# Kernel optimization log

Hardware: AMD Instinct MI355X
Metric: run time of the kernel (lower is better)

Reference implementation:

```python
import jax, jax.numpy as jnp
import numpy as np

B, T, C = 4, 2048, 1024
N_HEAD = 16
HEAD_DIM = C // N_HEAD


def setup_inputs() -> dict:
    key = jax.random.key(0)
    ks = jax.random.split(key, 5)
    s = 0.02
    return {
        "x": jax.random.normal(ks[0], (B, T, C), dtype=jnp.float32),
        "w_attn": jax.random.normal(ks[1], (C, 3 * C), dtype=jnp.float32) * s,
        "b_attn": jnp.zeros((3 * C,), dtype=jnp.float32),
        "w_proj": jax.random.normal(ks[2], (C, C), dtype=jnp.float32) * s,
        "b_proj": jnp.zeros((C,), dtype=jnp.float32),
    }


def reference(x, w_attn, b_attn, w_proj, b_proj):
    Bx, Tx, Cx = x.shape
    qkv = x @ w_attn + b_attn  # [B,T,3C]
    q, k, v = jnp.split(qkv, 3, axis=-1)
    # [B, H, T, D]
    q = q.reshape(Bx, Tx, N_HEAD, HEAD_DIM).transpose(0, 2, 1, 3)
    k = k.reshape(Bx, Tx, N_HEAD, HEAD_DIM).transpose(0, 2, 1, 3)
    v = v.reshape(Bx, Tx, N_HEAD, HEAD_DIM).transpose(0, 2, 1, 3)
    scale = 1.0 / np.sqrt(HEAD_DIM).astype(np.float32)
    att = jnp.einsum("bhqd,bhkd->bhqk", q, k) * scale  # [B,H,T,T]
    causal = jnp.tril(jnp.ones((Tx, Tx), dtype=bool))
    att = jnp.where(causal[None, None], att, jnp.float32(-jnp.inf))
    att = jax.nn.softmax(att, axis=-1)
    y = jnp.einsum("bhqk,bhkd->bhqd", att, v)  # [B,H,T,D]
    y = y.transpose(0, 2, 1, 3).reshape(Bx, Tx, Cx)
    return y @ w_proj + b_proj
```

## Files before the change

kernel.cpp:

```cpp
#include <hip/hip_runtime.h>
#include <hip/hip_bf16.h>

#define T_SEQ 2048
#define NHEAD 16
#define HDIM  64
#define CDIM  1024

typedef __attribute__((ext_vector_type(8))) short bf16x8;
typedef __attribute__((ext_vector_type(4))) short bf16x4;
typedef __attribute__((ext_vector_type(4))) float f32x4;

__device__ __forceinline__ unsigned short f2bf(float f) {
  union { __hip_bfloat16 h; unsigned short u; } c;
  c.h = __float2bfloat16(f);
  return c.u;
}

#define GLD16(g, l) __builtin_amdgcn_global_load_lds( \
  (const __attribute__((address_space(1))) void*)(g), \
  (__attribute__((address_space(3))) void*)(l), 16, 0, 0)

__global__ void cvt_bf16(const float* __restrict__ in, unsigned short* __restrict__ out, int n4) {
  const int i = blockIdx.x * 256 + threadIdx.x;
  if (i >= n4) return;
  const float4 v = ((const float4*)in)[i];
  ushort4 o;
  o.x = f2bf(v.x); o.y = f2bf(v.y); o.z = f2bf(v.z); o.w = f2bf(v.w);
  ((ushort4*)out)[i] = o;
}

__global__ void transpose_cvt(const float* __restrict__ in, unsigned short* __restrict__ out,
                              int R, int C) {
  __shared__ float tile[32][33];
  const int tx = threadIdx.x & 31, ty = threadIdx.x >> 5;
  const int c0 = blockIdx.x * 32, r0 = blockIdx.y * 32;
#pragma unroll
  for (int i = 0; i < 32; i += 8)
    tile[ty + i][tx] = in[(size_t)(r0 + ty + i) * C + c0 + tx];
  __syncthreads();
#pragma unroll
  for (int i = 0; i < 32; i += 8)
    out[(size_t)(c0 + ty + i) * R + r0 + tx] = f2bf(tile[tx][ty + i]);
}

template<int OUTF32>
__global__ __launch_bounds__(256, 2)
void gemm_bt(const unsigned short* __restrict__ A, const unsigned short* __restrict__ BT,
             const float* __restrict__ bias, void* __restrict__ outp,
             int M, int N, int K) {
  const int tid = threadIdx.x;
  const int w = tid >> 6, lane = tid & 63;
  const int lg = lane >> 4, l15 = lane & 15;
  const int wr = w >> 1, wc = w & 1;
  const int n0 = blockIdx.x * 128, m0 = blockIdx.y * 128;

  __shared__ unsigned short As[128 * 32];
  __shared__ unsigned short Bs[128 * 32];

  f32x4 acc[4][4] = {};

  for (int k0 = 0; k0 < K; k0 += 32) {
    __syncthreads();
#pragma unroll
    for (int i = 0; i < 2; ++i) {
      const int cb = i * 256 + w * 64;
      const int c  = cb + lane;
      const int row = c >> 2, slot = c & 3;
      GLD16(A  + (size_t)(m0 + row) * K + k0 + slot * 8, (char*)As + cb * 16);
      GLD16(BT + (size_t)(n0 + row) * K + k0 + slot * 8, (char*)Bs + cb * 16);
    }
    __syncthreads();
    bf16x8 af[4], bfr[4];
#pragma unroll
    for (int mt = 0; mt < 4; ++mt)
      af[mt] = *(const bf16x8*)&As[(wr * 64 + mt * 16 + l15) * 32 + lg * 8];
#pragma unroll
    for (int nt = 0; nt < 4; ++nt)
      bfr[nt] = *(const bf16x8*)&Bs[(wc * 64 + nt * 16 + l15) * 32 + lg * 8];
#pragma unroll
    for (int mt = 0; mt < 4; ++mt)
#pragma unroll
      for (int nt = 0; nt < 4; ++nt)
        acc[mt][nt] = __builtin_amdgcn_mfma_f32_16x16x32_bf16(af[mt], bfr[nt], acc[mt][nt], 0, 0, 0);
  }

#pragma unroll
  for (int mt = 0; mt < 4; ++mt) {
#pragma unroll
    for (int nt = 0; nt < 4; ++nt) {
      const int col = n0 + wc * 64 + nt * 16 + l15;
      const float bv = bias[col];
#pragma unroll
      for (int j = 0; j < 4; ++j) {
        const int row = m0 + wr * 64 + mt * 16 + lg * 4 + j;
        const float v = acc[mt][nt][j] + bv;
        if (OUTF32) ((float*)outp)[(size_t)row * N + col] = v;
        else ((unsigned short*)outp)[(size_t)row * N + col] = f2bf(v);
      }
    }
  }
}

#define EXPC 0.18033688f
__global__ __launch_bounds__(512, 4)
void attn_causal5(const unsigned short* __restrict__ qkv, unsigned short* __restrict__ att) {
  const int tid = threadIdx.x;
  const int w = tid >> 6, lane = tid & 63;
  const int lg = lane >> 4, l15 = lane & 15;

  const int fid = blockIdx.x;
  const int f2 = (fid & 7) * 64 + (fid >> 3);
  const int pair = f2 & 7, bh = f2 >> 3;
  const int b = bh >> 4, h = bh & 15;

  __shared__ unsigned short Kl[2][2][64][32];
  __shared__ unsigned short Vt[2][64][64];

  const unsigned short* base = qkv + (size_t)b * T_SEQ * 3072;

  auto STAGE_K = [&](int kv0, int buf) {
    const int c = tid;
    const int kc = c >> 8, slot = (c >> 2) & 63;
    const int s2 = (c & 3) ^ ((slot >> 1) & 3);
    const int v = (slot & 35) | ((slot & 8) << 1) | ((slot & 4) << 1) | ((slot & 16) >> 2);
    GLD16(base + (size_t)(kv0 + v) * 3072 + 1024 + h * 64 + kc * 32 + s2 * 8,
          (char*)&Kl[buf][0][0][0] + w * 1024);
  };

  bf16x4 vra, vrb;
  const int vkp = tid >> 4, vd4 = tid & 15;
  auto VLOAD = [&](int kv0) {
    const unsigned short* p = base + (size_t)(kv0 + 2 * vkp) * 3072 + 2048 + h * 64 + vd4 * 4;
    vra = *(const bf16x4*)p;
    vrb = *(const bf16x4*)(p + 3072);
  };
  auto VWRITE = [&](int buf) {
    const int ch = vkp >> 2, cl = (vkp & 3) * 2;
#pragma unroll
    for (int j = 0; j < 4; ++j) {
      const int r = vd4 * 4 + j;
      const unsigned int u = (unsigned short)vra[j] |
                             ((unsigned int)(unsigned short)vrb[j] << 16);
      *(unsigned int*)&Vt[buf][r][((ch ^ (r >> 3) ^ (r & 7)) << 3) + cl] = u;
    }
  };

  bf16x8 ones;
#pragma unroll
  for (int j = 0; j < 8; ++j) ones[j] = (short)0x3F80;

  for (int half = 0; half < 2; ++half) {
    const int qt = half ? (15 - pair) : pair;
    const int q0 = qt << 7;
    const int ntl = (qt + 1) << 1;
    const int qminS = __builtin_amdgcn_readfirstlane(q0 + w * 16);
    const int qme = qminS + l15;

    bf16x8 qf[2];
#pragma unroll
    for (int kc = 0; kc < 2; ++kc)
      qf[kc] = *(const bf16x8*)(base + (size_t)qme * 3072 + h * 64 + kc * 32 + lg * 8);

    f32x4 oacc[4] = {};
    f32x4 lsum = {};
    float m = -1e30f;

    STAGE_K(0, 0);
    VLOAD(0);
    VWRITE(0);
    __syncthreads();

    for (int t = 0; t < ntl; ++t) {
      const int cur = t & 1, nxt = cur ^ 1;
      const bool pf = (t + 1) < ntl;
      if (pf) { STAGE_K((t + 1) << 6, nxt); VLOAD((t + 1) << 6); }
      const int kv0 = t << 6;

      if (kv0 <= qminS + 15) {
        const int ksl = (lg ^ ((l15 >> 1) & 3)) * 8;
        f32x4 sc[4];
        __builtin_amdgcn_s_setprio(1);
#pragma unroll
        for (int kg = 0; kg < 4; ++kg) {
          f32x4 s = {};
#pragma unroll
          for (int kc = 0; kc < 2; ++kc) {
            bf16x8 kf = *(const bf16x8*)&Kl[cur][kc][kg * 16 + l15][ksl];
            s = __builtin_amdgcn_mfma_f32_16x16x32_bf16(kf, qf[kc], s, 0, 0, 0);
          }
          sc[kg] = s;
        }
        __builtin_amdgcn_s_setprio(0);

        float sv[4][4];
        if (kv0 + 63 > qminS) {
#pragma unroll
          for (int kg = 0; kg < 4; ++kg) {
            const int colb = kv0 + ((kg >> 1) << 5) + ((kg & 1) << 2) + lg * 8;
#pragma unroll
            for (int j = 0; j < 4; ++j)
              sv[kg][j] = (colb + j <= qme) ? sc[kg][j] : -1e30f;
          }
        } else {
#pragma unroll
          for (int kg = 0; kg < 4; ++kg)
#pragma unroll
            for (int j = 0; j < 4; ++j) sv[kg][j] = sc[kg][j];
        }

        float mx = -1e30f;
#pragma unroll
        for (int kg = 0; kg < 4; ++kg) {
          const float a = fmaxf(sv[kg][0], sv[kg][1]);
          const float c2 = fmaxf(sv[kg][2], sv[kg][3]);
          mx = fmaxf(mx, fmaxf(a, c2));
        }

        if (__any(mx > m + 55.4f)) {
          float mw = fmaxf(mx, __shfl_xor(mx, 16));
          mw = fmaxf(mw, __shfl_xor(mw, 32));
          const float mnew = fmaxf(m, mw);
          const float alc = exp2f((m - mnew) * EXPC);
          m = mnew;
          float alq[4];
#pragma unroll
          for (int j = 0; j < 4; ++j)
            alq[j] = __shfl(alc, (lane & 48) | (lg * 4 + j));
#pragma unroll
          for (int j = 0; j < 4; ++j) {
            lsum[j] *= alq[j];
#pragma unroll
            for (int dt = 0; dt < 4; ++dt) oacc[dt][j] *= alq[j];
          }
        }

        const float mc = m * EXPC;
        bf16x8 pa[2];
#pragma unroll
        for (int kg = 0; kg < 4; ++kg) {
          const int ks = kg >> 1, off = (kg & 1) * 4;
#pragma unroll
          for (int j = 0; j < 4; ++j) {
            const float p = exp2f(__fmaf_rn(sv[kg][j], EXPC, -mc));
            pa[ks][off + j] = (short)f2bf(p);
          }
        }

        __builtin_amdgcn_s_setprio(1);
        lsum = __builtin_amdgcn_mfma_f32_16x16x32_bf16(pa[0], ones, lsum, 0, 0, 0);
        lsum = __builtin_amdgcn_mfma_f32_16x16x32_bf16(pa[1], ones, lsum, 0, 0, 0);
#pragma unroll
        for (int dt = 0; dt < 4; ++dt) {
          f32x4 o = oacc[dt];
          const int d = dt * 16 + l15;
          const int gx = (d >> 3) ^ (d & 7);
#pragma unroll
          for (int ks = 0; ks < 2; ++ks) {
            bf16x8 vb = *(const bf16x8*)&Vt[cur][d][((ks * 4 + lg) ^ gx) << 3];
            o = __builtin_amdgcn_mfma_f32_16x16x32_bf16(pa[ks], vb, o, 0, 0, 0);
          }
          oacc[dt] = o;
        }
        __builtin_amdgcn_s_setprio(0);
      }

      if (pf) VWRITE(nxt);
      __syncthreads();
    }

#pragma unroll
    for (int dt = 0; dt < 4; ++dt)
#pragma unroll
      for (int j = 0; j < 4; ++j) {
        const int q = qminS + lg * 4 + j;
        att[(size_t)(b * T_SEQ + q) * CDIM + h * HDIM + dt * 16 + l15] =
            f2bf(oacc[dt][j] / lsum[j]);
      }
  }
}

extern "C" void kernel_launch(void* const* d_in, const int* in_sizes, int n_in,
                              void* d_out, int out_size, void* d_ws, size_t ws_size,
                              hipStream_t stream) {
  const float* x      = (const float*)d_in[0];
  const float* w_attn = (const float*)d_in[1];
  const float* b_attn = (const float*)d_in[2];
  const float* w_proj = (const float*)d_in[3];
  const float* b_proj = (const float*)d_in[4];

  char* ws = (char*)d_ws;
  unsigned short* xb  = (unsigned short*)(ws + 0);
  unsigned short* wat = (unsigned short*)(ws + 16777216);
  unsigned short* wpt = (unsigned short*)(ws + 23068672);
  unsigned short* qkv = (unsigned short*)(ws + 25165824);
  unsigned short* att = (unsigned short*)(ws + 75497472);

  cvt_bf16<<<8192, 256, 0, stream>>>(x, xb, 2097152);
  transpose_cvt<<<dim3(96, 32), 256, 0, stream>>>(w_attn, wat, 1024, 3072);
  transpose_cvt<<<dim3(32, 32), 256, 0, stream>>>(w_proj, wpt, 1024, 1024);
  gemm_bt<0><<<dim3(24, 64), 256, 0, stream>>>(xb, wat, b_attn, (void*)qkv, 8192, 3072, 1024);
  attn_causal5<<<dim3(512), 512, 0, stream>>>(qkv, att);
  gemm_bt<1><<<dim3(8, 64), 256, 0, stream>>>(att, wpt, b_proj, d_out, 8192, 1024, 1024);
}
```

Measured before the change: 187.6 us.

## Process two query row-tiles per wave in attention and swizzle GEMM block order

The attention kernel now runs 4 waves instead of 8, and each wave handles 32 query rows (two 16-row MFMA tiles). Each K and V fragment read from LDS is therefore reused for two MFMAs, and each thread stages twice as many K/V chunks. The GEMM remaps block indices with a stride-8 swizzle to improve L2 locality and raises its launch-bounds occupancy hint from 2 to 3. The trade-offs are more registers per wave and fewer waves per block to hide the softmax and load latency.

```diff
diff --git a/kernel.cpp b/kernel.cpp
--- a/kernel.cpp
+++ b/kernel.cpp
@@ -44,7 +44,7 @@
 }
 
 template<int OUTF32>
-__global__ __launch_bounds__(256, 2)
+__global__ __launch_bounds__(256, 3)
 void gemm_bt(const unsigned short* __restrict__ A, const unsigned short* __restrict__ BT,
              const float* __restrict__ bias, void* __restrict__ outp,
              int M, int N, int K) {
@@ -52,7 +52,11 @@
   const int w = tid >> 6, lane = tid & 63;
   const int lg = lane >> 4, l15 = lane & 15;
   const int wr = w >> 1, wc = w & 1;
-  const int n0 = blockIdx.x * 128, m0 = blockIdx.y * 128;
+
+  const int nb = gridDim.x * gridDim.y;
+  const int fid = blockIdx.y * gridDim.x + blockIdx.x;
+  const int swz = (fid & 7) * (nb >> 3) + (fid >> 3);
+  const int n0 = (swz % gridDim.x) * 128, m0 = (swz / gridDim.x) * 128;
 
   __shared__ unsigned short As[128 * 32];
   __shared__ unsigned short Bs[128 * 32];
@@ -102,8 +106,8 @@
 }
 
 #define EXPC 0.18033688f
-__global__ __launch_bounds__(512, 4)
-void attn_causal5(const unsigned short* __restrict__ qkv, unsigned short* __restrict__ att) {
+__global__ __launch_bounds__(256, 2)
+void attn_causal6(const unsigned short* __restrict__ qkv, unsigned short* __restrict__ att) {
   const int tid = threadIdx.x;
   const int w = tid >> 6, lane = tid & 63;
   const int lg = lane >> 4, l15 = lane & 15;
@@ -119,29 +123,39 @@
   const unsigned short* base = qkv + (size_t)b * T_SEQ * 3072;
 
   auto STAGE_K = [&](int kv0, int buf) {
-    const int c = tid;
-    const int kc = c >> 8, slot = (c >> 2) & 63;
-    const int s2 = (c & 3) ^ ((slot >> 1) & 3);
-    const int v = (slot & 35) | ((slot & 8) << 1) | ((slot & 4) << 1) | ((slot & 16) >> 2);
-    GLD16(base + (size_t)(kv0 + v) * 3072 + 1024 + h * 64 + kc * 32 + s2 * 8,
-          (char*)&Kl[buf][0][0][0] + w * 1024);
+#pragma unroll
+    for (int i = 0; i < 2; ++i) {
+      const int c = i * 256 + tid;
+      const int kc = c >> 8, slot = (c >> 2) & 63;
+      const int s2 = (c & 3) ^ ((slot >> 1) & 3);
+      const int v = (slot & 35) | ((slot & 8) << 1) | ((slot & 4) << 1) | ((slot & 16) >> 2);
+      GLD16(base + (size_t)(kv0 + v) * 3072 + 1024 + h * 64 + kc * 32 + s2 * 8,
+            (char*)&Kl[buf][0][0][0] + i * 4096 + w * 1024);
+    }
   };
 
-  bf16x4 vra, vrb;
-  const int vkp = tid >> 4, vd4 = tid & 15;
+  bf16x4 vra[2], vrb[2];
+  const int vkp0 = tid >> 4, vd4 = tid & 15;
   auto VLOAD = [&](int kv0) {
-    const unsigned short* p = base + (size_t)(kv0 + 2 * vkp) * 3072 + 2048 + h * 64 + vd4 * 4;
-    vra = *(const bf16x4*)p;
-    vrb = *(const bf16x4*)(p + 3072);
+#pragma unroll
+    for (int u = 0; u < 2; ++u) {
+      const unsigned short* p = base + (size_t)(kv0 + 2 * vkp0 + u * 32) * 3072 + 2048 + h * 64 + vd4 * 4;
+      vra[u] = *(const bf16x4*)p;
+      vrb[u] = *(const bf16x4*)(p + 3072);
+    }
   };
   auto VWRITE = [&](int buf) {
-    const int ch = vkp >> 2, cl = (vkp & 3) * 2;
-#pragma unroll
-    for (int j = 0; j < 4; ++j) {
-      const int r = vd4 * 4 + j;
-      const unsigned int u = (unsigned short)vra[j] |
-                             ((unsigned int)(unsigned short)vrb[j] << 16);
-      *(unsigned int*)&Vt[buf][r][((ch ^ (r >> 3) ^ (r & 7)) << 3) + cl] = u;
+#pragma unroll
+    for (int u = 0; u < 2; ++u) {
+      const int vkp = vkp0 + u * 16;
+      const int ch = vkp >> 2, cl = (vkp & 3) * 2;
+#pragma unroll
+      for (int j = 0; j < 4; ++j) {
+        const int r = vd4 * 4 + j;
+        const unsigned int pk = (unsigned short)vra[u][j] |
+                                ((unsigned int)(unsigned short)vrb[u][j] << 16);
+        *(unsigned int*)&Vt[buf][r][((ch ^ (r >> 3) ^ (r & 7)) << 3) + cl] = pk;
+      }
     }
   };
 
@@ -153,17 +167,19 @@
     const int qt = half ? (15 - pair) : pair;
     const int q0 = qt << 7;
     const int ntl = (qt + 1) << 1;
-    const int qminS = __builtin_amdgcn_readfirstlane(q0 + w * 16);
-    const int qme = qminS + l15;
-
-    bf16x8 qf[2];
-#pragma unroll
-    for (int kc = 0; kc < 2; ++kc)
-      qf[kc] = *(const bf16x8*)(base + (size_t)qme * 3072 + h * 64 + kc * 32 + lg * 8);
-
-    f32x4 oacc[4] = {};
-    f32x4 lsum = {};
-    float m = -1e30f;
+    const int qminS = __builtin_amdgcn_readfirstlane(q0 + w * 32);
+
+    bf16x8 qf[2][2];
+#pragma unroll
+    for (int qr = 0; qr < 2; ++qr)
+#pragma unroll
+      for (int kc = 0; kc < 2; ++kc)
+        qf[qr][kc] = *(const bf16x8*)(base + (size_t)(qminS + qr * 16 + l15) * 3072 +
+                                      h * 64 + kc * 32 + lg * 8);
+
+    f32x4 oacc[2][4] = {};
+    f32x4 lsum[2] = {};
+    float m[2] = {-1e30f, -1e30f};
 
     STAGE_K(0, 0);
     VLOAD(0);
@@ -176,90 +192,104 @@
       if (pf) { STAGE_K((t + 1) << 6, nxt); VLOAD((t + 1) << 6); }
       const int kv0 = t << 6;
 
-      if (kv0 <= qminS + 15) {
+      if (kv0 <= qminS + 31) {
         const int ksl = (lg ^ ((l15 >> 1) & 3)) * 8;
-        f32x4 sc[4];
+        f32x4 sc[2][4];
         __builtin_amdgcn_s_setprio(1);
 #pragma unroll
         for (int kg = 0; kg < 4; ++kg) {
-          f32x4 s = {};
+          f32x4 s0 = {}, s1 = {};
 #pragma unroll
           for (int kc = 0; kc < 2; ++kc) {
             bf16x8 kf = *(const bf16x8*)&Kl[cur][kc][kg * 16 + l15][ksl];
-            s = __builtin_amdgcn_mfma_f32_16x16x32_bf16(kf, qf[kc], s, 0, 0, 0);
-          }
-          sc[kg] = s;
+            s0 = __builtin_amdgcn_mfma_f32_16x16x32_bf16(kf, qf[0][kc], s0, 0, 0, 0);
+            s1 = __builtin_amdgcn_mfma_f32_16x16x32_bf16(kf, qf[1][kc], s1, 0, 0, 0);
+          }
+          sc[0][kg] = s0; sc[1][kg] = s1;
         }
         __builtin_amdgcn_s_setprio(0);
 
-        float sv[4][4];
         if (kv0 + 63 > qminS) {
 #pragma unroll
+          for (int qr = 0; qr < 2; ++qr) {
+            const int qme = qminS + qr * 16 + l15;
+#pragma unroll
+            for (int kg = 0; kg < 4; ++kg) {
+              const int colb = kv0 + ((kg >> 1) << 5) + ((kg & 1) << 2) + lg * 8;
+#pragma unroll
+              for (int j = 0; j < 4; ++j)
+                if (colb + j > qme) sc[qr][kg][j] = -1e30f;
+            }
+          }
+        }
+
+        float mx[2];
+#pragma unroll
+        for (int qr = 0; qr < 2; ++qr) {
+          float m1 = -1e30f;
+#pragma unroll
           for (int kg = 0; kg < 4; ++kg) {
-            const int colb = kv0 + ((kg >> 1) << 5) + ((kg & 1) << 2) + lg * 8;
+            const float a = fmaxf(sc[qr][kg][0], sc[qr][kg][1]);
+            const float c2 = fmaxf(sc[qr][kg][2], sc[qr][kg][3]);
+            m1 = fmaxf(m1, fmaxf(a, c2));
+          }
+          mx[qr] = m1;
+        }
+
+        if (__any(fmaxf(mx[0] - m[0], mx[1] - m[1]) > 55.4f)) {
+#pragma unroll
+          for (int qr = 0; qr < 2; ++qr) {
+            float mw = fmaxf(mx[qr], __shfl_xor(mx[qr], 16));
+            mw = fmaxf(mw, __shfl_xor(mw, 32));
+            const float mnew = fmaxf(m[qr], mw);
+            const float alc = exp2f((m[qr] - mnew) * EXPC);
+            m[qr] = mnew;
+            float alq[4];
 #pragma unroll
             for (int j = 0; j < 4; ++j)
-              sv[kg][j] = (colb + j <= qme) ? sc[kg][j] : -1e30f;
-          }
-        } else {
-#pragma unroll
-          for (int kg = 0; kg < 4; ++kg)
-#pragma unroll
-            for (int j = 0; j < 4; ++j) sv[kg][j] = sc[kg][j];
-        }
-
-        float mx = -1e30f;
-#pragma unroll
-        for (int kg = 0; kg < 4; ++kg) {
-          const float a = fmaxf(sv[kg][0], sv[kg][1]);
-          const float c2 = fmaxf(sv[kg][2], sv[kg][3]);
-          mx = fmaxf(mx, fmaxf(a, c2));
-        }
-
-        if (__any(mx > m + 55.4f)) {
-          float mw = fmaxf(mx, __shfl_xor(mx, 16));
-          mw = fmaxf(mw, __shfl_xor(mw, 32));
-          const float mnew = fmaxf(m, mw);
-          const float alc = exp2f((m - mnew) * EXPC);
-          m = mnew;
-          float alq[4];
-#pragma unroll
-          for (int j = 0; j < 4; ++j)
-            alq[j] = __shfl(alc, (lane & 48) | (lg * 4 + j));
-#pragma unroll
-          for (int j = 0; j < 4; ++j) {
-            lsum[j] *= alq[j];
-#pragma unroll
-            for (int dt = 0; dt < 4; ++dt) oacc[dt][j] *= alq[j];
-          }
-        }
-
-        const float mc = m * EXPC;
-        bf16x8 pa[2];
-#pragma unroll
-        for (int kg = 0; kg < 4; ++kg) {
-          const int ks = kg >> 1, off = (kg & 1) * 4;
-#pragma unroll
-          for (int j = 0; j < 4; ++j) {
-            const float p = exp2f(__fmaf_rn(sv[kg][j], EXPC, -mc));
-            pa[ks][off + j] = (short)f2bf(p);
+              alq[j] = __shfl(alc, (lane & 48) | (lg * 4 + j));
+#pragma unroll
+            for (int j = 0; j < 4; ++j) {
+              lsum[qr][j] *= alq[j];
+#pragma unroll
+              for (int dt = 0; dt < 4; ++dt) oacc[qr][dt][j] *= alq[j];
+            }
+          }
+        }
+
+        bf16x8 pa[2][2];
+#pragma unroll
+        for (int qr = 0; qr < 2; ++qr) {
+          const float mc = m[qr] * EXPC;
+#pragma unroll
+          for (int kg = 0; kg < 4; ++kg) {
+            const int ks = kg >> 1, off = (kg & 1) * 4;
+#pragma unroll
+            for (int j = 0; j < 4; ++j) {
+              const float p = exp2f(__fmaf_rn(sc[qr][kg][j], EXPC, -mc));
+              pa[qr][ks][off + j] = (short)f2bf(p);
+            }
           }
         }
 
         __builtin_amdgcn_s_setprio(1);
-        lsum = __builtin_amdgcn_mfma_f32_16x16x32_bf16(pa[0], ones, lsum, 0, 0, 0);
-        lsum = __builtin_amdgcn_mfma_f32_16x16x32_bf16(pa[1], ones, lsum, 0, 0, 0);
+#pragma unroll
+        for (int qr = 0; qr < 2; ++qr) {
+          lsum[qr] = __builtin_amdgcn_mfma_f32_16x16x32_bf16(pa[qr][0], ones, lsum[qr], 0, 0, 0);
+          lsum[qr] = __builtin_amdgcn_mfma_f32_16x16x32_bf16(pa[qr][1], ones, lsum[qr], 0, 0, 0);
+        }
 #pragma unroll
         for (int dt = 0; dt < 4; ++dt) {
-          f32x4 o = oacc[dt];
           const int d = dt * 16 + l15;
           const int gx = (d >> 3) ^ (d & 7);
+          f32x4 o0 = oacc[0][dt], o1 = oacc[1][dt];
 #pragma unroll
           for (int ks = 0; ks < 2; ++ks) {
             bf16x8 vb = *(const bf16x8*)&Vt[cur][d][((ks * 4 + lg) ^ gx) << 3];
-            o = __builtin_amdgcn_mfma_f32_16x16x32_bf16(pa[ks], vb, o, 0, 0, 0);
-          }
-          oacc[dt] = o;
+            o0 = __builtin_amdgcn_mfma_f32_16x16x32_bf16(pa[0][ks], vb, o0, 0, 0, 0);
+            o1 = __builtin_amdgcn_mfma_f32_16x16x32_bf16(pa[1][ks], vb, o1, 0, 0, 0);
+          }
+          oacc[0][dt] = o0; oacc[1][dt] = o1;
         }
         __builtin_amdgcn_s_setprio(0);
       }
@@ -269,13 +299,15 @@
     }
 
 #pragma unroll
-    for (int dt = 0; dt < 4; ++dt)
-#pragma unroll
-      for (int j = 0; j < 4; ++j) {
-        const int q = qminS + lg * 4 + j;
-        att[(size_t)(b * T_SEQ + q) * CDIM + h * HDIM + dt * 16 + l15] =
-            f2bf(oacc[dt][j] / lsum[j]);
-      }
+    for (int qr = 0; qr < 2; ++qr)
+#pragma unroll
+      for (int dt = 0; dt < 4; ++dt)
+#pragma unroll
+        for (int j = 0; j < 4; ++j) {
+          const int q = qminS + qr * 16 + lg * 4 + j;
+          att[(size_t)(b * T_SEQ + q) * CDIM + h * HDIM + dt * 16 + l15] =
+              f2bf(oacc[qr][dt][j] / lsum[qr][j]);
+        }
   }
 }
 
@@ -299,6 +331,6 @@
   transpose_cvt<<<dim3(96, 32), 256, 0, stream>>>(w_attn, wat, 1024, 3072);
   transpose_cvt<<<dim3(32, 32), 256, 0, stream>>>(w_proj, wpt, 1024, 1024);
   gemm_bt<0><<<dim3(24, 64), 256, 0, stream>>>(xb, wat, b_attn, (void*)qkv, 8192, 3072, 1024);
-  attn_causal5<<<dim3(512), 512, 0, stream>>>(qkv, att);
+  attn_causal6<<<dim3(512), 256, 0, stream>>>(qkv, att);
   gemm_bt<1><<<dim3(8, 64), 256, 0, stream>>>(att, wpt, b_proj, d_out, 8192, 1024, 1024);
 }
```

Result: no change. 188.2 us (+0.3%).

## Widen attention KV tile to 128, swizzle GEMM block order, raise occupancy

Applied to the files above, without the earlier changes.

The attention kernel now processes 128 KV positions per iteration instead of 64. This halves the loop trips and barriers and drops the per-tile skip check. The K and V LDS buffers are doubled, with an adjusted swizzle, and the causal mask applies only on the diagonal tile. Some waves now compute fully masked blocks, and the larger LDS footprint may limit occupancy. Separately, the GEMM remaps block indices for L2 locality, raises its launch-bounds occupancy hint to 3, and the final normalization uses a reciprocal instead of a divide.

```diff
diff --git a/kernel.cpp b/kernel.cpp
--- a/kernel.cpp
+++ b/kernel.cpp
@@ -44,7 +44,7 @@
 }
 
 template<int OUTF32>
-__global__ __launch_bounds__(256, 2)
+__global__ __launch_bounds__(256, 3)
 void gemm_bt(const unsigned short* __restrict__ A, const unsigned short* __restrict__ BT,
              const float* __restrict__ bias, void* __restrict__ outp,
              int M, int N, int K) {
@@ -52,7 +52,11 @@
   const int w = tid >> 6, lane = tid & 63;
   const int lg = lane >> 4, l15 = lane & 15;
   const int wr = w >> 1, wc = w & 1;
-  const int n0 = blockIdx.x * 128, m0 = blockIdx.y * 128;
+
+  const int nb = gridDim.x * gridDim.y;
+  const int fid = blockIdx.y * gridDim.x + blockIdx.x;
+  const int swz = (fid & 7) * (nb >> 3) + (fid >> 3);
+  const int n0 = (swz % gridDim.x) * 128, m0 = (swz / gridDim.x) * 128;
 
   __shared__ unsigned short As[128 * 32];
   __shared__ unsigned short Bs[128 * 32];
@@ -103,7 +107,7 @@
 
 #define EXPC 0.18033688f
 __global__ __launch_bounds__(512, 4)
-void attn_causal5(const unsigned short* __restrict__ qkv, unsigned short* __restrict__ att) {
+void attn_causal9(const unsigned short* __restrict__ qkv, unsigned short* __restrict__ att) {
   const int tid = threadIdx.x;
   const int w = tid >> 6, lane = tid & 63;
   const int lg = lane >> 4, l15 = lane & 15;
@@ -113,35 +117,46 @@
   const int pair = f2 & 7, bh = f2 >> 3;
   const int b = bh >> 4, h = bh & 15;
 
-  __shared__ unsigned short Kl[2][2][64][32];
-  __shared__ unsigned short Vt[2][64][64];
+  __shared__ unsigned short Kl[2][2][128][32];
+  __shared__ unsigned short Vt[2][64][128];
 
   const unsigned short* base = qkv + (size_t)b * T_SEQ * 3072;
 
   auto STAGE_K = [&](int kv0, int buf) {
-    const int c = tid;
-    const int kc = c >> 8, slot = (c >> 2) & 63;
-    const int s2 = (c & 3) ^ ((slot >> 1) & 3);
-    const int v = (slot & 35) | ((slot & 8) << 1) | ((slot & 4) << 1) | ((slot & 16) >> 2);
-    GLD16(base + (size_t)(kv0 + v) * 3072 + 1024 + h * 64 + kc * 32 + s2 * 8,
-          (char*)&Kl[buf][0][0][0] + w * 1024);
+#pragma unroll
+    for (int i = 0; i < 2; ++i) {
+      const int c = i * 512 + tid;
+      const int kc = c >> 9, slot = (c >> 2) & 127;
+      const int s2 = (c & 3) ^ ((slot >> 1) & 3);
+      const int v = (slot & 99) | ((slot & 8) << 1) | ((slot & 4) << 1) | ((slot & 16) >> 2);
+      GLD16(base + (size_t)(kv0 + v) * 3072 + 1024 + h * 64 + kc * 32 + s2 * 8,
+            (char*)&Kl[buf][0][0][0] + i * 8192 + w * 1024);
+    }
   };
 
-  bf16x4 vra, vrb;
-  const int vkp = tid >> 4, vd4 = tid & 15;
+  bf16x4 vra[2], vrb[2];
+  const int vkp0 = tid >> 4, vd4 = tid & 15;
   auto VLOAD = [&](int kv0) {
-    const unsigned short* p = base + (size_t)(kv0 + 2 * vkp) * 3072 + 2048 + h * 64 + vd4 * 4;
-    vra = *(const bf16x4*)p;
-    vrb = *(const bf16x4*)(p + 3072);
+#pragma unroll
+    for (int uu = 0; uu < 2; ++uu) {
+      const unsigned short* p = base + (size_t)(kv0 + 2 * (vkp0 + 32 * uu)) * 3072 + 2048 + h * 64 + vd4 * 4;
+      vra[uu] = *(const bf16x4*)p;
+      vrb[uu] = *(const bf16x4*)(p + 3072);
+    }
   };
   auto VWRITE = [&](int buf) {
-    const int ch = vkp >> 2, cl = (vkp & 3) * 2;
-#pragma unroll
-    for (int j = 0; j < 4; ++j) {
-      const int r = vd4 * 4 + j;
-      const unsigned int u = (unsigned short)vra[j] |
-                             ((unsigned int)(unsigned short)vrb[j] << 16);
-      *(unsigned int*)&Vt[buf][r][((ch ^ (r >> 3) ^ (r & 7)) << 3) + cl] = u;
+#pragma unroll
+    for (int uu = 0; uu < 2; ++uu) {
+      const int p2 = vkp0 + 32 * uu;
+      const int ch = p2 >> 2, cl = (p2 & 3) * 2;
+#pragma unroll
+      for (int j = 0; j < 4; ++j) {
+        const int r = vd4 * 4 + j;
+        const int phys = (ch & 8) | ((ch ^ (r >> 3) ^ (r & 7)) & 7);
+        const unsigned int pk = (unsigned short)vra[uu][j] |
+                                ((unsigned int)(unsigned short)vrb[uu][j] << 16);
+        *(unsigned int*)&Vt[buf][r][phys * 8 + cl] = pk;
+      }
     }
   };
 
@@ -152,7 +167,7 @@
   for (int half = 0; half < 2; ++half) {
     const int qt = half ? (15 - pair) : pair;
     const int q0 = qt << 7;
-    const int ntl = (qt + 1) << 1;
+    const int ntl = qt + 1;
     const int qminS = __builtin_amdgcn_readfirstlane(q0 + w * 16);
     const int qme = qminS + l15;
 
@@ -173,108 +188,106 @@
     for (int t = 0; t < ntl; ++t) {
       const int cur = t & 1, nxt = cur ^ 1;
       const bool pf = (t + 1) < ntl;
-      if (pf) { STAGE_K((t + 1) << 6, nxt); VLOAD((t + 1) << 6); }
-      const int kv0 = t << 6;
-
-      if (kv0 <= qminS + 15) {
-        const int ksl = (lg ^ ((l15 >> 1) & 3)) * 8;
-        f32x4 sc[4];
-        __builtin_amdgcn_s_setprio(1);
-#pragma unroll
-        for (int kg = 0; kg < 4; ++kg) {
-          f32x4 s = {};
-#pragma unroll
-          for (int kc = 0; kc < 2; ++kc) {
-            bf16x8 kf = *(const bf16x8*)&Kl[cur][kc][kg * 16 + l15][ksl];
-            s = __builtin_amdgcn_mfma_f32_16x16x32_bf16(kf, qf[kc], s, 0, 0, 0);
-          }
-          sc[kg] = s;
-        }
-        __builtin_amdgcn_s_setprio(0);
-
-        float sv[4][4];
-        if (kv0 + 63 > qminS) {
-#pragma unroll
-          for (int kg = 0; kg < 4; ++kg) {
-            const int colb = kv0 + ((kg >> 1) << 5) + ((kg & 1) << 2) + lg * 8;
-#pragma unroll
-            for (int j = 0; j < 4; ++j)
-              sv[kg][j] = (colb + j <= qme) ? sc[kg][j] : -1e30f;
-          }
-        } else {
-#pragma unroll
-          for (int kg = 0; kg < 4; ++kg)
-#pragma unroll
-            for (int j = 0; j < 4; ++j) sv[kg][j] = sc[kg][j];
-        }
-
-        float mx = -1e30f;
-#pragma unroll
-        for (int kg = 0; kg < 4; ++kg) {
-          const float a = fmaxf(sv[kg][0], sv[kg][1]);
-          const float c2 = fmaxf(sv[kg][2], sv[kg][3]);
-          mx = fmaxf(mx, fmaxf(a, c2));
-        }
-
-        if (__any(mx > m + 55.4f)) {
-          float mw = fmaxf(mx, __shfl_xor(mx, 16));
-          mw = fmaxf(mw, __shfl_xor(mw, 32));
-          const float mnew = fmaxf(m, mw);
-          const float alc = exp2f((m - mnew) * EXPC);
-          m = mnew;
-          float alq[4];
+      if (pf) { STAGE_K((t + 1) << 7, nxt); VLOAD((t + 1) << 7); }
+      const int kv0 = t << 7;
+
+      const int ksl = (lg ^ ((l15 >> 1) & 3)) * 8;
+      f32x4 sc[8];
+      __builtin_amdgcn_s_setprio(1);
+#pragma unroll
+      for (int kg = 0; kg < 8; ++kg) {
+        f32x4 s = {};
+#pragma unroll
+        for (int kc = 0; kc < 2; ++kc) {
+          bf16x8 kf = *(const bf16x8*)&Kl[cur][kc][kg * 16 + l15][ksl];
+          s = __builtin_amdgcn_mfma_f32_16x16x32_bf16(kf, qf[kc], s, 0, 0, 0);
+        }
+        sc[kg] = s;
+      }
+      __builtin_amdgcn_s_setprio(0);
+
+      if (t == qt) {
+#pragma unroll
+        for (int kg = 0; kg < 8; ++kg) {
+          const int colb = kv0 + ((kg >> 1) << 5) + ((kg & 1) << 2) + lg * 8;
 #pragma unroll
           for (int j = 0; j < 4; ++j)
-            alq[j] = __shfl(alc, (lane & 48) | (lg * 4 + j));
-#pragma unroll
-          for (int j = 0; j < 4; ++j) {
-            lsum[j] *= alq[j];
-#pragma unroll
-            for (int dt = 0; dt < 4; ++dt) oacc[dt][j] *= alq[j];
-          }
-        }
-
-        const float mc = m * EXPC;
-        bf16x8 pa[2];
-#pragma unroll
-        for (int kg = 0; kg < 4; ++kg) {
-          const int ks = kg >> 1, off = (kg & 1) * 4;
-#pragma unroll
-          for (int j = 0; j < 4; ++j) {
-            const float p = exp2f(__fmaf_rn(sv[kg][j], EXPC, -mc));
-            pa[ks][off + j] = (short)f2bf(p);
-          }
-        }
-
-        __builtin_amdgcn_s_setprio(1);
-        lsum = __builtin_amdgcn_mfma_f32_16x16x32_bf16(pa[0], ones, lsum, 0, 0, 0);
-        lsum = __builtin_amdgcn_mfma_f32_16x16x32_bf16(pa[1], ones, lsum, 0, 0, 0);
-#pragma unroll
-        for (int dt = 0; dt < 4; ++dt) {
-          f32x4 o = oacc[dt];
-          const int d = dt * 16 + l15;
-          const int gx = (d >> 3) ^ (d & 7);
-#pragma unroll
-          for (int ks = 0; ks < 2; ++ks) {
-            bf16x8 vb = *(const bf16x8*)&Vt[cur][d][((ks * 4 + lg) ^ gx) << 3];
-            o = __builtin_amdgcn_mfma_f32_16x16x32_bf16(pa[ks], vb, o, 0, 0, 0);
-          }
-          oacc[dt] = o;
-        }
-        __builtin_amdgcn_s_setprio(0);
-      }
+            if (colb + j > qme) sc[kg][j] = -1e30f;
+        }
+      }
+
+      float mx = -1e30f;
+#pragma unroll
+      for (int kg = 0; kg < 8; ++kg) {
+        const float a = fmaxf(sc[kg][0], sc[kg][1]);
+        const float c2 = fmaxf(sc[kg][2], sc[kg][3]);
+        mx = fmaxf(mx, fmaxf(a, c2));
+      }
+
+      if (__any(mx > m + 55.4f)) {
+        float mw = fmaxf(mx, __shfl_xor(mx, 16));
+        mw = fmaxf(mw, __shfl_xor(mw, 32));
+        const float mnew = fmaxf(m, mw);
+        const float alc = exp2f((m - mnew) * EXPC);
+        m = mnew;
+        float alq[4];
+#pragma unroll
+        for (int j = 0; j < 4; ++j)
+          alq[j] = __shfl(alc, (lane & 48) | (lg * 4 + j));
+#pragma unroll
+        for (int j = 0; j < 4; ++j) {
+          lsum[j] *= alq[j];
+#pragma unroll
+          for (int dt = 0; dt < 4; ++dt) oacc[dt][j] *= alq[j];
+        }
+      }
+
+      const float mc = m * EXPC;
+      bf16x8 pa[4];
+#pragma unroll
+      for (int kg = 0; kg < 8; ++kg) {
+        const int ks = kg >> 1, off = (kg & 1) * 4;
+#pragma unroll
+        for (int j = 0; j < 4; ++j) {
+          const float p = exp2f(__fmaf_rn(sc[kg][j], EXPC, -mc));
+          pa[ks][off + j] = (short)f2bf(p);
+        }
+      }
+
+      __builtin_amdgcn_s_setprio(1);
+#pragma unroll
+      for (int ks = 0; ks < 4; ++ks)
+        lsum = __builtin_amdgcn_mfma_f32_16x16x32_bf16(pa[ks], ones, lsum, 0, 0, 0);
+#pragma unroll
+      for (int dt = 0; dt < 4; ++dt) {
+        f32x4 o = oacc[dt];
+        const int d = dt * 16 + l15;
+        const int gx = (d >> 3) ^ (d & 7);
+#pragma unroll
+        for (int ks = 0; ks < 4; ++ks) {
+          const int slot = ks * 4 + lg;
+          const int phys = (slot & 8) | ((slot ^ gx) & 7);
+          bf16x8 vb = *(const bf16x8*)&Vt[cur][d][phys * 8];
+          o = __builtin_amdgcn_mfma_f32_16x16x32_bf16(pa[ks], vb, o, 0, 0, 0);
+        }
+        oacc[dt] = o;
+      }
+      __builtin_amdgcn_s_setprio(0);
 
       if (pf) VWRITE(nxt);
       __syncthreads();
     }
 
+    f32x4 inv;
+#pragma unroll
+    for (int j = 0; j < 4; ++j) inv[j] = __builtin_amdgcn_rcpf(lsum[j]);
 #pragma unroll
     for (int dt = 0; dt < 4; ++dt)
 #pragma unroll
       for (int j = 0; j < 4; ++j) {
         const int q = qminS + lg * 4 + j;
         att[(size_t)(b * T_SEQ + q) * CDIM + h * HDIM + dt * 16 + l15] =
-            f2bf(oacc[dt][j] / lsum[j]);
+            f2bf(oacc[dt][j] * inv[j]);
       }
   }
 }
@@ -299,6 +312,6 @@
   transpose_cvt<<<dim3(96, 32), 256, 0, stream>>>(w_attn, wat, 1024, 3072);
   transpose_cvt<<<dim3(32, 32), 256, 0, stream>>>(w_proj, wpt, 1024, 1024);
   gemm_bt<0><<<dim3(24, 64), 256, 0, stream>>>(xb, wat, b_attn, (void*)qkv, 8192, 3072, 1024);
-  attn_causal5<<<dim3(512), 512, 0, stream>>>(qkv, att);
+  attn_causal9<<<dim3(512), 512, 0, stream>>>(qkv, att);
   gemm_bt<1><<<dim3(8, 64), 256, 0, stream>>>(att, wpt, b_proj, d_out, 8192, 1024, 1024);
 }
```

After: 183.4 us. 2.2% less time.
